# Kernel tuning notes

Measured on AMD Instinct MI355X. Metric: run time of the kernel, lower is better.

Reference implementation:

```python
import jax, jax.numpy as jnp
import numpy as np

DIM = 1024
NH = 16
HD = DIM // NH  # 64
WINDOW = 8      # window_size; flash window=(WINDOW-1, -1) with causal=True
EPS_NORM = 1e-6


def _rmsnorm(h, w):
    # RMSNorm over last dim (full model dim, applied before head split)
    return h * jax.lax.rsqrt(jnp.mean(h * h, axis=-1, keepdims=True) + EPS_NORM) * w


def _rope(h, cos, sin):
    # h: [bv, L, NH, HD]; cos/sin: [L, HD//2]; torch view-as-complex pairs adjacent elems
    hr = h[..., 0::2]
    hi = h[..., 1::2]
    c = cos[None, :, None, :]
    s = sin[None, :, None, :]
    out_r = hr * c - hi * s
    out_i = hr * s + hi * c
    return jnp.stack([out_r, out_i], axis=-1).reshape(h.shape)


def setup_inputs() -> dict:
    key = jax.random.key(0)
    ks = jax.random.split(key, 8)
    bv, f, nlt = 1, 16, 1472
    b = bv * f
    L = f * nlt
    wscale = DIM ** -0.5
    x = jax.random.normal(ks[0], (b, nlt, DIM), jnp.float32)
    # standard RoPE tables, base 10000, d//2 frequencies
    pos = jnp.arange(L, dtype=jnp.float32)[:, None]
    inv_freq = 1.0 / (10000.0 ** (jnp.arange(HD // 2, dtype=jnp.float32) / (HD // 2)))
    ang = pos * inv_freq[None, :]
    inp = {
        'x': x,
        'freqs_cos': jnp.cos(ang),
        'freqs_sin': jnp.sin(ang),
        'q_w': jax.random.normal(ks[1], (DIM, DIM), jnp.float32) * wscale,
        'q_b': jnp.zeros((DIM,), jnp.float32),
        'k_w': jax.random.normal(ks[2], (DIM, DIM), jnp.float32) * wscale,
        'k_b': jnp.zeros((DIM,), jnp.float32),
        'v_w': jax.random.normal(ks[3], (DIM, DIM), jnp.float32) * wscale,
        'v_b': jnp.zeros((DIM,), jnp.float32),
        'o_w': jax.random.normal(ks[4], (DIM, DIM), jnp.float32) * wscale,
        'o_b': jnp.zeros((DIM,), jnp.float32),
        'norm_q_w': jnp.ones((DIM,), jnp.float32),
        'norm_k_w': jnp.ones((DIM,), jnp.float32),
        'bv': 1,
        'f': 16,
        'nlt': 1472,
    }
    return inp


def reference(x, freqs_cos, freqs_sin, q_w, q_b, k_w, k_b, v_w, v_b, o_w, o_b,
              norm_q_w, norm_k_w, bv, f, nlt):
    b, s = x.shape[:2]  # b = bv*f, s = nlt
    q = _rmsnorm(x @ q_w.T + q_b, norm_q_w)
    k = _rmsnorm(x @ k_w.T + k_b, norm_k_w)
    v = (x @ v_w.T + v_b).reshape(bv, f, s, NH, HD)
    # RoPE over flattened (frame, token) positions
    q4 = q.reshape(bv, f * s, NH, HD)
    k4 = k.reshape(bv, f * s, NH, HD)
    qr = _rope(q4, freqs_cos, freqs_sin)
    kr = _rope(k4, freqs_cos, freqs_sin)
    # temporal layout: [bv*nlt, f, NH, HD] (attend over frames per latent token)
    qr = qr.reshape(bv, f, s, NH, HD).transpose(0, 2, 1, 3, 4).reshape(bv * s, f, NH, HD)
    kr = kr.reshape(bv, f, s, NH, HD).transpose(0, 2, 1, 3, 4).reshape(bv * s, f, NH, HD)
    vr = v.transpose(0, 2, 1, 3, 4).reshape(bv * s, f, NH, HD)
    # causal sliding-window mask over frames: j <= i and i - j < WINDOW
    fi = jnp.arange(f)
    mask = (fi[None, :] <= fi[:, None]) & (fi[:, None] - fi[None, :] < WINDOW)  # [f, f]
    scores = jnp.einsum('bqhd,bkhd->bhqk', qr, kr) / np.float32(np.sqrt(HD))
    scores = jnp.where(mask[None, None], scores, jnp.float32(-1e30))
    attn = jax.nn.softmax(scores, axis=-1)
    o = jnp.einsum('bhqk,bkhd->bqhd', attn, vr)  # [bv*nlt, f, NH, HD]
    o = o.reshape(bv, s, f, NH, HD).transpose(0, 2, 1, 3, 4).reshape(bv * f, s, DIM)
    return o @ o_w.T + o_b
```

## Files before the change

### kernel.cpp

```cpp
#include <hip/hip_runtime.h>
#include <hip/hip_bf16.h>
#include <math.h>

typedef __bf16 bf16;
typedef bf16 bf16x8 __attribute__((ext_vector_type(8)));
typedef bf16 bf16x4 __attribute__((ext_vector_type(4)));
typedef float f32x4 __attribute__((ext_vector_type(4)));

#define NFRM 16
#define SEQ  1472
#define TOK  (NFRM * SEQ)
#define DIM_ 1024
#define NH_  16
#define HD_  64
#define KROW 1032


__device__ __forceinline__ void load_lds_16B(const void* g, void* l) {
  __builtin_amdgcn_global_load_lds(
      (const __attribute__((address_space(1))) unsigned int*)g,
      (__attribute__((address_space(3))) unsigned int*)l,
      16, 0, 0);
}

__global__ __launch_bounds__(256) void cvt_bf16(const float* __restrict__ s,
                                                bf16* __restrict__ d, int n) {
  size_t i = ((size_t)blockIdx.x * 256 + threadIdx.x) * 8;
  if (i >= (size_t)n) return;
  f32x4 a = *(const f32x4*)(s + i);
  f32x4 b = *(const f32x4*)(s + i + 4);
  bf16x8 o;
  o[0] = (bf16)a[0]; o[1] = (bf16)a[1]; o[2] = (bf16)a[2]; o[3] = (bf16)a[3];
  o[4] = (bf16)b[0]; o[5] = (bf16)b[1]; o[6] = (bf16)b[2]; o[7] = (bf16)b[3];
  *(bf16x8*)(d + i) = o;
}

__global__ __launch_bounds__(256) void cvt_w4(
    const float* __restrict__ w0, const float* __restrict__ w1,
    const float* __restrict__ w2, const float* __restrict__ w3,
    bf16* __restrict__ d0, bf16* __restrict__ d1,
    bf16* __restrict__ d2, bf16* __restrict__ d3) {
  const int z = blockIdx.y;
  const float* s = (z == 0) ? w0 : (z == 1) ? w1 : (z == 2) ? w2 : w3;
  bf16* d       = (z == 0) ? d0 : (z == 1) ? d1 : (z == 2) ? d2 : d3;
  size_t i = ((size_t)blockIdx.x * 256 + threadIdx.x) * 8;
  f32x4 a = *(const f32x4*)(s + i);
  f32x4 b = *(const f32x4*)(s + i + 4);
  bf16x8 o;
  o[0] = (bf16)a[0]; o[1] = (bf16)a[1]; o[2] = (bf16)a[2]; o[3] = (bf16)a[3];
  o[4] = (bf16)b[0]; o[5] = (bf16)b[1]; o[6] = (bf16)b[2]; o[7] = (bf16)b[3];
  *(bf16x8*)(d + i) = o;
}

template <typename OutT, int AMAP>
__device__ __forceinline__ void gemm_body(const bf16* __restrict__ A,
                                          const bf16* __restrict__ B,
                                          const float* __restrict__ bias,
                                          OutT* __restrict__ C,
                                          bf16* As, bf16* Bs) {
  const int tid  = threadIdx.x;
  const int wave = tid >> 6;
  const int lane = tid & 63;
  const size_t am0 = (size_t)blockIdx.x * 128;
  const size_t bn0 = (size_t)blockIdx.y * 128;

  f32x4 acc[4][4];
#pragma unroll
  for (int i = 0; i < 4; ++i)
#pragma unroll
    for (int j = 0; j < 4; ++j) {
      f32x4 z = {0.f, 0.f, 0.f, 0.f};
      acc[i][j] = z;
    }

  const int wm   = (wave >> 1) * 64;
  const int wn   = (wave & 1) * 64;
  const int frow = lane & 15;
  const int fko  = (lane >> 4) * 8;

  const int r0 = (wave * 64 + lane) >> 2;
  const int kc = (lane & 3) * 8;
  size_t ar0 = am0 + r0, ar1 = am0 + r0 + 64;
  if (AMAP == 1) {
    ar0 = (ar0 & 15) * (size_t)SEQ + (ar0 >> 4);
    ar1 = (ar1 & 15) * (size_t)SEQ + (ar1 >> 4);
  } else if (AMAP == 2) {
    const unsigned f0 = (unsigned)ar0 / SEQ, f1 = (unsigned)ar1 / SEQ;
    ar0 = ((unsigned)ar0 - f0 * SEQ) * 16ull + f0;
    ar1 = ((unsigned)ar1 - f1 * SEQ) * 16ull + f1;
  }
  const bf16* pa0 = A + ar0 * DIM_ + kc;
  const bf16* pa1 = A + ar1 * DIM_ + kc;
  const bf16* pb0 = B + (bn0 + r0) * DIM_ + kc;
  const bf16* pb1 = B + (bn0 + r0 + 64) * DIM_ + kc;
  const int cb0 = wave * 64, cb1 = 256 + wave * 64;

  for (int k0 = 0; k0 < DIM_; k0 += 32) {
    load_lds_16B(pa0 + k0, As + cb0 * 8);
    load_lds_16B(pb0 + k0, Bs + cb0 * 8);
    load_lds_16B(pa1 + k0, As + cb1 * 8);
    load_lds_16B(pb1 + k0, Bs + cb1 * 8);
    __syncthreads();
    bf16x8 af[4], bfv[4];
#pragma unroll
    for (int i = 0; i < 4; ++i)
      af[i] = *(const bf16x8*)(As + (wm + i * 16 + frow) * 32 + fko);
#pragma unroll
    for (int j = 0; j < 4; ++j)
      bfv[j] = *(const bf16x8*)(Bs + (wn + j * 16 + frow) * 32 + fko);
#pragma unroll
    for (int i = 0; i < 4; ++i)
#pragma unroll
      for (int j = 0; j < 4; ++j)
        acc[i][j] = __builtin_amdgcn_mfma_f32_16x16x32_bf16(af[i], bfv[j],
                                                            acc[i][j], 0, 0, 0);
    __syncthreads();
  }

  const int cl = lane & 15;
  const int rq = (lane >> 4) * 4;
#pragma unroll
  for (int i = 0; i < 4; ++i)
#pragma unroll
    for (int j = 0; j < 4; ++j) {
      const int nc   = (int)bn0 + wn + j * 16 + cl;
      const float bb = bias[nc];
#pragma unroll
      for (int r = 0; r < 4; ++r) {
        const size_t mr = am0 + wm + i * 16 + rq + r;
        C[mr * DIM_ + nc] = (OutT)(acc[i][j][r] + bb);
      }
    }
}

__global__ __launch_bounds__(256) void gemm_qkv(
    const bf16* __restrict__ A,
    const bf16* __restrict__ Bq, const bf16* __restrict__ Bk,
    const bf16* __restrict__ Bv,
    const float* __restrict__ bq, const float* __restrict__ bk,
    const float* __restrict__ bv,
    bf16* __restrict__ Cq, bf16* __restrict__ Ck, bf16* __restrict__ Cv) {
  __shared__ __align__(16) bf16 As[128 * 32];
  __shared__ __align__(16) bf16 Bs[128 * 32];
  const int z = blockIdx.z;
  const bf16* B    = (z == 0) ? Bq : (z == 1) ? Bk : Bv;
  const float* bia = (z == 0) ? bq : (z == 1) ? bk : bv;
  bf16* C          = (z == 0) ? Cq : (z == 1) ? Ck : Cv;
  gemm_body<bf16, 1>(A, B, bia, C, As, Bs);
}

__global__ __launch_bounds__(256) void gemm_out(
    const bf16* __restrict__ A, const bf16* __restrict__ B,
    const float* __restrict__ bias, float* __restrict__ C) {
  __shared__ __align__(16) bf16 As[128 * 32];
  __shared__ __align__(16) bf16 Bs[128 * 32];
  gemm_body<float, 2>(A, B, bias, C, As, Bs);
}

__global__ __launch_bounds__(256) void norm_rope(
    bf16* __restrict__ q, bf16* __restrict__ k,
    const float* __restrict__ nqw, const float* __restrict__ nkw,
    const float* __restrict__ fcos, const float* __restrict__ fsin) {
  const int lane = threadIdx.x & 63, wave = threadIdx.x >> 6;
  const size_t row  = (size_t)blockIdx.x * 4 + wave;
  const size_t base = row * DIM_;
  const size_t pos  = (row & 15) * (size_t)SEQ + (row >> 4);
  const int e0 = lane * 16;
  const int j0 = (lane & 3) * 8;

  float cs[8], sn[8];
#pragma unroll
  for (int i = 0; i < 8; ++i) {
    cs[i] = fcos[pos * 32 + j0 + i];
    sn[i] = fsin[pos * 32 + j0 + i];
  }

  bf16x8 qa = *(const bf16x8*)(q + base + e0);
  bf16x8 qb = *(const bf16x8*)(q + base + e0 + 8);
  bf16x8 ka = *(const bf16x8*)(k + base + e0);
  bf16x8 kb = *(const bf16x8*)(k + base + e0 + 8);

  float xq[16], xk[16];
#pragma unroll
  for (int i = 0; i < 8; ++i) {
    xq[i] = (float)qa[i]; xq[8 + i] = (float)qb[i];
    xk[i] = (float)ka[i]; xk[8 + i] = (float)kb[i];
  }
  float sq = 0.f, sk = 0.f;
#pragma unroll
  for (int i = 0; i < 16; ++i) { sq += xq[i] * xq[i]; sk += xk[i] * xk[i]; }
#pragma unroll
  for (int off = 32; off > 0; off >>= 1) {
    sq += __shfl_xor(sq, off);
    sk += __shfl_xor(sk, off);
  }
  const float rq = rsqrtf(sq * (1.0f / 1024.0f) + 1e-6f);
  const float rk = rsqrtf(sk * (1.0f / 1024.0f) + 1e-6f);
#pragma unroll
  for (int i = 0; i < 16; ++i) {
    xq[i] *= rq * nqw[e0 + i];
    xk[i] *= rk * nkw[e0 + i];
  }
  bf16x8 oa, ob, oc, od;
#pragma unroll
  for (int p = 0; p < 8; ++p) {
    const float c = cs[p], s = sn[p];
    const float q0 = xq[2 * p], q1 = xq[2 * p + 1];
    const float k0 = xk[2 * p], k1 = xk[2 * p + 1];
    const float qr = q0 * c - q1 * s, qi = q0 * s + q1 * c;
    const float kr = k0 * c - k1 * s, ki = k0 * s + k1 * c;
    if (p < 4) { oa[2 * p] = (bf16)qr; oa[2 * p + 1] = (bf16)qi;
                 oc[2 * p] = (bf16)kr; oc[2 * p + 1] = (bf16)ki; }
    else       { ob[2 * p - 8] = (bf16)qr; ob[2 * p - 7] = (bf16)qi;
                 od[2 * p - 8] = (bf16)kr; od[2 * p - 7] = (bf16)ki; }
  }
  *(bf16x8*)(q + base + e0)     = oa;
  *(bf16x8*)(q + base + e0 + 8) = ob;
  *(bf16x8*)(k + base + e0)     = oc;
  *(bf16x8*)(k + base + e0 + 8) = od;
}

__global__ __launch_bounds__(512, 4) void attn_win(
    const bf16* __restrict__ q, const bf16* __restrict__ k,
    const bf16* __restrict__ v, bf16* __restrict__ o) {
  __shared__ __align__(16) bf16 ks[16 * KROW];
  __shared__ __align__(16) bf16 vs[16 * KROW];
  __shared__ __align__(16) bf16 ps[16 * 256];
  const int t    = blockIdx.x;
  const int tid  = threadIdx.x;
  const int wave = tid >> 6, lane = tid & 63;
  const size_t tb = (size_t)t * (16 * DIM_);

#pragma unroll
  for (int i = 0; i < 4; ++i) {
    const int j = wave * 4 + i;
    const int r = j >> 1, half = j & 1;
    const size_t g = tb + (size_t)r * DIM_ + half * 512 + lane * 8;
    load_lds_16B(k + g, ks + r * KROW + half * 512);
    load_lds_16B(v + g, vs + r * KROW + half * 512);
  }
  __syncthreads();

  const int fl  = lane & 15;
  const int kq  = (lane >> 4) * 8;
#pragma unroll
  for (int hh = 0; hh < 2; ++hh) {
    const int h = wave * 2 + hh;
    const size_t qg = tb + (size_t)fl * DIM_ + h * HD_ + kq;
    bf16x8 aq0 = *(const bf16x8*)(q + qg);
    bf16x8 aq1 = *(const bf16x8*)(q + qg + 32);
    const int ko = fl * KROW + h * HD_ + kq;
    bf16x8 bk0 = *(const bf16x8*)(ks + ko);
    bf16x8 bk1 = *(const bf16x8*)(ks + ko + 32);
    f32x4 sc = {0.f, 0.f, 0.f, 0.f};
    sc = __builtin_amdgcn_mfma_f32_16x16x32_bf16(aq0, bk0, sc, 0, 0, 0);
    sc = __builtin_amdgcn_mfma_f32_16x16x32_bf16(aq1, bk1, sc, 0, 0, 0);
#pragma unroll
    for (int r = 0; r < 4; ++r) {
      const int row = (lane >> 4) * 4 + r;
      const bool valid = (fl <= row) && (row - fl < 8);
      float s = valid ? sc[r] * 0.125f : -1e30f;
      float m = s;
#pragma unroll
      for (int off = 8; off > 0; off >>= 1) m = fmaxf(m, __shfl_xor(m, off));
      const float e = __expf(s - m);
      float su = e;
#pragma unroll
      for (int off = 8; off > 0; off >>= 1) su += __shfl_xor(su, off);
      ps[h * 256 + row * 16 + fl] = (bf16)(e / su);
    }
  }
  __syncthreads();

  const int h3 = tid >> 5;
  const int dc = (tid >> 2) & 7;
  const int fg = tid & 3;
  bf16x8 pr[8];
#pragma unroll
  for (int i = 0; i < 4; ++i) {
    pr[2 * i]     = *(const bf16x8*)(ps + h3 * 256 + (fg * 4 + i) * 16);
    pr[2 * i + 1] = *(const bf16x8*)(ps + h3 * 256 + (fg * 4 + i) * 16 + 8);
  }
  float acc[4][8];
#pragma unroll
  for (int i = 0; i < 4; ++i)
#pragma unroll
    for (int d = 0; d < 8; ++d) acc[i][d] = 0.f;

  const bf16* vb = vs + h3 * HD_ + dc * 8;
#pragma unroll
  for (int fk2 = 0; fk2 < 16; ++fk2) {
    bf16x8 vv8 = *(const bf16x8*)(vb + fk2 * KROW);
    float vf[8];
#pragma unroll
    for (int d = 0; d < 8; ++d) vf[d] = (float)vv8[d];
#pragma unroll
    for (int i = 0; i < 4; ++i) {
      const float pp = (float)((fk2 < 8) ? pr[2 * i][fk2] : pr[2 * i + 1][fk2 - 8]);
#pragma unroll
      for (int d = 0; d < 8; ++d) acc[i][d] += pp * vf[d];
    }
  }
#pragma unroll
  for (int i = 0; i < 4; ++i) {
    bf16x8 ov;
#pragma unroll
    for (int d = 0; d < 8; ++d) ov[d] = (bf16)acc[i][d];
    *(bf16x8*)(o + tb + (size_t)(fg * 4 + i) * DIM_ + h3 * HD_ + dc * 8) = ov;
  }
}

extern "C" void kernel_launch(void* const* d_in, const int* in_sizes, int n_in,
                              void* d_out, int out_size, void* d_ws,
                              size_t ws_size, hipStream_t stream) {
  const float* x    = (const float*)d_in[0];
  const float* fcos = (const float*)d_in[1];
  const float* fsin = (const float*)d_in[2];
  const float* q_w  = (const float*)d_in[3];
  const float* q_b  = (const float*)d_in[4];
  const float* k_w  = (const float*)d_in[5];
  const float* k_b  = (const float*)d_in[6];
  const float* v_w  = (const float*)d_in[7];
  const float* v_b  = (const float*)d_in[8];
  const float* o_w  = (const float*)d_in[9];
  const float* o_b  = (const float*)d_in[10];
  const float* nqw  = (const float*)d_in[11];
  const float* nkw  = (const float*)d_in[12];
  float* out = (float*)d_out;

  char* ws = (char*)d_ws;
  const size_t SZ  = (size_t)TOK * DIM_ * 2;
  const size_t WSZ = (size_t)DIM_ * DIM_ * 2;
  bf16* xb = (bf16*)(ws);
  bf16* wq = (bf16*)(ws + SZ);
  bf16* wk = (bf16*)(ws + SZ + WSZ);
  bf16* wv = (bf16*)(ws + SZ + 2 * WSZ);
  bf16* wo = (bf16*)(ws + SZ + 3 * WSZ);
  bf16* qq = (bf16*)(ws + SZ + 4 * WSZ);
  bf16* kk = (bf16*)(ws + SZ + 4 * WSZ + SZ);
  bf16* vv = (bf16*)(ws + SZ + 4 * WSZ + 2 * SZ);
  bf16* om = xb;

  const int NTOT = TOK * DIM_;
  const int NW   = DIM_ * DIM_;

  cvt_bf16<<<NTOT / 2048, 256, 0, stream>>>(x, xb, NTOT);
  cvt_w4<<<dim3(NW / 2048, 4), 256, 0, stream>>>(q_w, k_w, v_w, o_w,
                                                 wq, wk, wv, wo);

  dim3 gq(TOK / 128, DIM_ / 128, 3);
  gemm_qkv<<<gq, 256, 0, stream>>>(xb, wq, wk, wv, q_b, k_b, v_b, qq, kk, vv);

  norm_rope<<<TOK / 4, 256, 0, stream>>>(qq, kk, nqw, nkw, fcos, fsin);

  attn_win<<<SEQ, 512, 0, stream>>>(qq, kk, vv, om);

  gemm_out<<<dim3(TOK / 128, DIM_ / 128), 256, 0, stream>>>(om, wo, o_b, out);
}
```

Baseline: 553.2 us.

## Rewrite GEMMs with 256x256 tiles, double-buffered swizzled LDS and async prefetch

Replaces the 128x128, single-buffered GEMM body with a 256x256 tile, 512-thread block that uses a 64-wide K step. It double-buffers LDS through global_load_lds prefetch with explicit vmcnt waits, XOR-swizzles LDS rows to avoid bank conflicts, and raises MFMA priority with setprio. The aim is to cut global traffic per FLOP and hide load latency behind MFMA work, at the cost of 128KB of LDS per block and higher register pressure. The grid shrinks to 368 blocks for the out GEMM, which may underfill the CUs.

```diff
diff --git a/kernel.cpp b/kernel.cpp
--- a/kernel.cpp
+++ b/kernel.cpp
@@ -53,108 +53,155 @@
 }
 
 template <typename OutT, int AMAP>
-__device__ __forceinline__ void gemm_body(const bf16* __restrict__ A,
-                                          const bf16* __restrict__ B,
-                                          const float* __restrict__ bias,
-                                          OutT* __restrict__ C,
-                                          bf16* As, bf16* Bs) {
+__device__ __forceinline__ void gemm256_body(const bf16* __restrict__ A,
+                                             const bf16* __restrict__ B,
+                                             const float* __restrict__ bias,
+                                             OutT* __restrict__ C,
+                                             bf16* lds) {
   const int tid  = threadIdx.x;
-  const int wave = tid >> 6;
+  const int w    = tid >> 6;
   const int lane = tid & 63;
-  const size_t am0 = (size_t)blockIdx.x * 128;
-  const size_t bn0 = (size_t)blockIdx.y * 128;
-
-  f32x4 acc[4][4];
-#pragma unroll
-  for (int i = 0; i < 4; ++i)
+  const int am0  = blockIdx.x * 256;
+  const int bn0  = blockIdx.y * 256;
+
+  const int rstep = w * 8 + (lane >> 3);
+  const int jsrc  = ((lane & 7) ^ ((lane >> 3) & 7)) * 8;
+  const int arb[4] = {0, 128, 64, 192};
+  const bf16* srcp[8];
+  int dstoff[8];
+#pragma unroll
+  for (int s = 0; s < 4; ++s) {
+    srcp[s]   = B + (size_t)(bn0 + s * 64 + rstep) * DIM_ + jsrc;
+    dstoff[s] = 32768 + s * 8192 + w * 1024;
+    int R = am0 + arb[s] + rstep;
+    size_t ar;
+    if (AMAP == 1)      ar = (size_t)(R & 15) * SEQ + (R >> 4);
+    else if (AMAP == 2) { unsigned f = (unsigned)R / SEQ;
+                          ar = (size_t)(R - (int)f * SEQ) * 16 + f; }
+    else                 ar = (size_t)R;
+    srcp[4 + s]   = A + ar * DIM_ + jsrc;
+    dstoff[4 + s] = arb[s] * 128 + w * 1024;
+  }
+
+  const int wr   = w >> 2;
+  const int wc   = w & 3;
+  const int frow = lane & 15;
+  const int g    = lane >> 4;
+  const int sw   = (frow & 7) << 4;
+  const int e0   = (g * 16) ^ sw;
+  const int e1   = (g * 16 + 64) ^ sw;
+  const int aA   = (wr * 128 + frow) * 128;
+  const int bB   = 32768 + (wc * 64 + frow) * 128;
+
+  f32x4 acc[8][4];
+#pragma unroll
+  for (int i = 0; i < 8; ++i)
 #pragma unroll
     for (int j = 0; j < 4; ++j) {
       f32x4 z = {0.f, 0.f, 0.f, 0.f};
       acc[i][j] = z;
     }
 
-  const int wm   = (wave >> 1) * 64;
-  const int wn   = (wave & 1) * 64;
-  const int frow = lane & 15;
-  const int fko  = (lane >> 4) * 8;
-
-  const int r0 = (wave * 64 + lane) >> 2;
-  const int kc = (lane & 3) * 8;
-  size_t ar0 = am0 + r0, ar1 = am0 + r0 + 64;
-  if (AMAP == 1) {
-    ar0 = (ar0 & 15) * (size_t)SEQ + (ar0 >> 4);
-    ar1 = (ar1 & 15) * (size_t)SEQ + (ar1 >> 4);
-  } else if (AMAP == 2) {
-    const unsigned f0 = (unsigned)ar0 / SEQ, f1 = (unsigned)ar1 / SEQ;
-    ar0 = ((unsigned)ar0 - f0 * SEQ) * 16ull + f0;
-    ar1 = ((unsigned)ar1 - f1 * SEQ) * 16ull + f1;
-  }
-  const bf16* pa0 = A + ar0 * DIM_ + kc;
-  const bf16* pa1 = A + ar1 * DIM_ + kc;
-  const bf16* pb0 = B + (bn0 + r0) * DIM_ + kc;
-  const bf16* pb1 = B + (bn0 + r0 + 64) * DIM_ + kc;
-  const int cb0 = wave * 64, cb1 = 256 + wave * 64;
-
-  for (int k0 = 0; k0 < DIM_; k0 += 32) {
-    load_lds_16B(pa0 + k0, As + cb0 * 8);
-    load_lds_16B(pb0 + k0, Bs + cb0 * 8);
-    load_lds_16B(pa1 + k0, As + cb1 * 8);
-    load_lds_16B(pb1 + k0, Bs + cb1 * 8);
-    __syncthreads();
-    bf16x8 af[4], bfv[4];
-#pragma unroll
-    for (int i = 0; i < 4; ++i)
-      af[i] = *(const bf16x8*)(As + (wm + i * 16 + frow) * 32 + fko);
-#pragma unroll
-    for (int j = 0; j < 4; ++j)
-      bfv[j] = *(const bf16x8*)(Bs + (wn + j * 16 + frow) * 32 + fko);
-#pragma unroll
-    for (int i = 0; i < 4; ++i)
-#pragma unroll
-      for (int j = 0; j < 4; ++j)
-        acc[i][j] = __builtin_amdgcn_mfma_f32_16x16x32_bf16(af[i], bfv[j],
-                                                            acc[i][j], 0, 0, 0);
-    __syncthreads();
+  char* ldsc = (char*)lds;
+
+#pragma unroll
+  for (int s = 0; s < 8; ++s) load_lds_16B(srcp[s], ldsc + dstoff[s]);
+
+#pragma unroll 1
+  for (int it = 0; it < 8; ++it) {
+#pragma unroll
+    for (int half = 0; half < 2; ++half) {
+      const int kt   = it * 2 + half;
+      const int cur  = half ? 65536 : 0;
+      const int nxt  = half ? 0 : 65536;
+      const int kpre = (kt < 15) ? (kt + 1) * 64 : 15 * 64;
+
+      asm volatile("s_waitcnt vmcnt(2)" ::: "memory");
+      asm volatile("s_barrier" ::: "memory");
+#pragma unroll
+      for (int s = 0; s < 4; ++s)
+        load_lds_16B(srcp[s] + kpre, ldsc + nxt + dstoff[s]);
+
+      bf16x8 bfv[4][2];
+#pragma unroll
+      for (int j = 0; j < 4; ++j) {
+        bfv[j][0] = *(const bf16x8*)(ldsc + cur + bB + j * 2048 + e0);
+        bfv[j][1] = *(const bf16x8*)(ldsc + cur + bB + j * 2048 + e1);
+      }
+
+#pragma unroll
+      for (int p = 0; p < 4; ++p) {
+        if (p == 1) {
+          load_lds_16B(srcp[4] + kpre, ldsc + nxt + dstoff[4]);
+          load_lds_16B(srcp[5] + kpre, ldsc + nxt + dstoff[5]);
+        }
+        if (p == 2) {
+          asm volatile("s_waitcnt vmcnt(6)" ::: "memory");
+          asm volatile("s_barrier" ::: "memory");
+          load_lds_16B(srcp[6] + kpre, ldsc + nxt + dstoff[6]);
+          load_lds_16B(srcp[7] + kpre, ldsc + nxt + dstoff[7]);
+        }
+        bf16x8 af[2][2];
+#pragma unroll
+        for (int ii = 0; ii < 2; ++ii) {
+          const int i = p * 2 + ii;
+          af[ii][0] = *(const bf16x8*)(ldsc + cur + aA + i * 2048 + e0);
+          af[ii][1] = *(const bf16x8*)(ldsc + cur + aA + i * 2048 + e1);
+        }
+        __builtin_amdgcn_s_setprio(1);
+#pragma unroll
+        for (int ii = 0; ii < 2; ++ii) {
+          const int i = p * 2 + ii;
+#pragma unroll
+          for (int j = 0; j < 4; ++j) {
+            acc[i][j] = __builtin_amdgcn_mfma_f32_16x16x32_bf16(
+                af[ii][0], bfv[j][0], acc[i][j], 0, 0, 0);
+            acc[i][j] = __builtin_amdgcn_mfma_f32_16x16x32_bf16(
+                af[ii][1], bfv[j][1], acc[i][j], 0, 0, 0);
+          }
+        }
+        __builtin_amdgcn_s_setprio(0);
+      }
+    }
   }
 
   const int cl = lane & 15;
-  const int rq = (lane >> 4) * 4;
-#pragma unroll
-  for (int i = 0; i < 4; ++i)
-#pragma unroll
-    for (int j = 0; j < 4; ++j) {
-      const int nc   = (int)bn0 + wn + j * 16 + cl;
-      const float bb = bias[nc];
+  const int rq = g * 4;
+#pragma unroll
+  for (int j = 0; j < 4; ++j) {
+    const int nc   = bn0 + wc * 64 + j * 16 + cl;
+    const float bb = bias[nc];
+#pragma unroll
+    for (int i = 0; i < 8; ++i) {
 #pragma unroll
       for (int r = 0; r < 4; ++r) {
-        const size_t mr = am0 + wm + i * 16 + rq + r;
+        const size_t mr = (size_t)am0 + wr * 128 + i * 16 + rq + r;
         C[mr * DIM_ + nc] = (OutT)(acc[i][j][r] + bb);
       }
     }
-}
-
-__global__ __launch_bounds__(256) void gemm_qkv(
+  }
+}
+
+__global__ __launch_bounds__(512, 2) void gemm_qkv(
     const bf16* __restrict__ A,
     const bf16* __restrict__ Bq, const bf16* __restrict__ Bk,
     const bf16* __restrict__ Bv,
     const float* __restrict__ bq, const float* __restrict__ bk,
     const float* __restrict__ bv,
     bf16* __restrict__ Cq, bf16* __restrict__ Ck, bf16* __restrict__ Cv) {
-  __shared__ __align__(16) bf16 As[128 * 32];
-  __shared__ __align__(16) bf16 Bs[128 * 32];
+  __shared__ __align__(16) bf16 lds[65536];
   const int z = blockIdx.z;
   const bf16* B    = (z == 0) ? Bq : (z == 1) ? Bk : Bv;
   const float* bia = (z == 0) ? bq : (z == 1) ? bk : bv;
   bf16* C          = (z == 0) ? Cq : (z == 1) ? Ck : Cv;
-  gemm_body<bf16, 1>(A, B, bia, C, As, Bs);
-}
-
-__global__ __launch_bounds__(256) void gemm_out(
+  gemm256_body<bf16, 1>(A, B, bia, C, lds);
+}
+
+__global__ __launch_bounds__(512, 2) void gemm_out(
     const bf16* __restrict__ A, const bf16* __restrict__ B,
     const float* __restrict__ bias, float* __restrict__ C) {
-  __shared__ __align__(16) bf16 As[128 * 32];
-  __shared__ __align__(16) bf16 Bs[128 * 32];
-  gemm_body<float, 2>(A, B, bias, C, As, Bs);
+  __shared__ __align__(16) bf16 lds[65536];
+  gemm256_body<float, 2>(A, B, bias, C, lds);
 }
 
 __global__ __launch_bounds__(256) void norm_rope(
@@ -348,12 +395,12 @@
   cvt_w4<<<dim3(NW / 2048, 4), 256, 0, stream>>>(q_w, k_w, v_w, o_w,
                                                  wq, wk, wv, wo);
 
-  dim3 gq(TOK / 128, DIM_ / 128, 3);
-  gemm_qkv<<<gq, 256, 0, stream>>>(xb, wq, wk, wv, q_b, k_b, v_b, qq, kk, vv);
+  dim3 gq(TOK / 256, DIM_ / 256, 3);
+  gemm_qkv<<<gq, 512, 0, stream>>>(xb, wq, wk, wv, q_b, k_b, v_b, qq, kk, vv);
 
   norm_rope<<<TOK / 4, 256, 0, stream>>>(qq, kk, nqw, nkw, fcos, fsin);
 
   attn_win<<<SEQ, 512, 0, stream>>>(qq, kk, vv, om);
 
-  gemm_out<<<dim3(TOK / 128, DIM_ / 128), 256, 0, stream>>>(om, wo, o_b, out);
-}
+  gemm_out<<<dim3(TOK / 256, DIM_ / 256), 512, 0, stream>>>(om, wo, o_b, out);
+}
```

Result: no change. 551.5 us (-0.3%).
